# Kernel optimization log

Hardware: AMD Instinct MI355X
Metric: run time of the kernel (lower is better)

## Reference

```python
import jax, jax.numpy as jnp
import numpy as np

H = 256
NUM_CONVS = 4
NUM_GRAPHS = 1024
N_PER_GRAPH = 32
ORDER = 3
NUM_TYPES = 22  # len(utils.BOND_TYPES)
NUM_NOISE_LEVEL = 50
ANNEAL_POWER = 2.0


def _build_graph():
    # Chain molecules extended to order-3 neighbors (mimics extend_graph on a path graph):
    # for |i-j| in [1,ORDER]: edge_order=|i-j|, edge_type = bond type if order 1 else NUM_TYPES+order-1.
    n = N_PER_GRAPH
    i, j = np.meshgrid(np.arange(n), np.arange(n), indexing='ij')
    dist = np.abs(i - j)
    mask = (dist >= 1) & (dist <= ORDER)
    src_l, dst_l, eo = i[mask], j[mask], dist[mask]
    offs = np.arange(NUM_GRAPHS)[:, None] * n
    src = (src_l[None, :] + offs).reshape(-1)
    dst = (dst_l[None, :] + offs).reshape(-1)
    edge_order = np.tile(eo, NUM_GRAPHS)
    rng = np.random.default_rng(0)
    bond_t = rng.integers(1, 5, size=edge_order.shape)
    edge_type = np.where(edge_order == 1, bond_t, NUM_TYPES + edge_order - 1)
    node2graph = np.repeat(np.arange(NUM_GRAPHS), n)
    return src, dst, edge_type, node2graph


def setup_inputs() -> dict:
    key = jax.random.key(0)
    ks = jax.random.split(key, 24)
    src, dst, edge_type, node2graph = _build_graph()
    N, E = node2graph.shape[0], src.shape[0]
    w = lambda k, s: (jax.random.normal(k, s, jnp.float32) * 0.05)
    sigmas = jnp.asarray(np.exp(np.linspace(np.log(10.0), np.log(0.01), NUM_NOISE_LEVEL)), dtype=jnp.float32)
    return {
        'atom_type': jnp.asarray(np.random.default_rng(1).integers(0, 100, N), jnp.int32),
        'edge_index': jnp.asarray(np.stack([src, dst]), jnp.int32),
        'edge_type': jnp.asarray(edge_type, jnp.int32),
        'node2graph': jnp.asarray(node2graph, jnp.int32),
        'noise_level': jax.random.randint(ks[0], (NUM_GRAPHS,), 0, NUM_NOISE_LEVEL, jnp.int32),
        'pos': jax.random.normal(ks[1], (N, 3), jnp.float32) * 3.0,
        'd_noise': jax.random.normal(ks[2], (E, 1), jnp.float32),
        'sigmas': sigmas,
        'node_emb': w(ks[3], (100, H)), 'edge_emb': w(ks[4], (100, H)),
        'in_W1': w(ks[5], (1, H)), 'in_b1': w(ks[6], (H,)),
        'in_W2': w(ks[7], (H, H)), 'in_b2': w(ks[8], (H,)),
        'gin_W1': w(ks[9], (NUM_CONVS, H, H)), 'gin_b1': w(ks[10], (NUM_CONVS, H)),
        'gin_W2': w(ks[11], (NUM_CONVS, H, H)), 'gin_b2': w(ks[12], (NUM_CONVS, H)),
        'out_W1': w(ks[13], (2 * H, H)), 'out_b1': w(ks[14], (H,)),
        'out_W2': w(ks[15], (H, H // 2)), 'out_b2': w(ks[16], (H // 2,)),
        'out_W3': w(ks[17], (H // 2, 1)), 'out_b3': w(ks[18], (1,)),
    }


def reference(atom_type, edge_index, edge_type, node2graph, noise_level,
              pos, d_noise, sigmas, node_emb, edge_emb,
              in_W1, in_b1, in_W2, in_b2,
              gin_W1, gin_b1, gin_W2, gin_b2,
              out_W1, out_b1, out_W2, out_b2, out_W3, out_b3):
    N = pos.shape[0]
    G = noise_level.shape[0]
    row, col = edge_index[0], edge_index[1]
    edge2graph = node2graph[row]                                  # [E]
    d = jnp.linalg.norm(pos[row] - pos[col], axis=-1, keepdims=True)  # [E,1]
    used_sigmas = sigmas[noise_level][edge2graph][:, None]        # [E,1]
    perturbed_d = d + d_noise * used_sigmas
    target = -(perturbed_d - d) / used_sigmas ** 2
    # embeddings + input MLP (Linear-relu-Linear)
    node_attr = node_emb[atom_type]                               # [N,H]
    d_emb = jax.nn.relu(perturbed_d @ in_W1 + in_b1) @ in_W2 + in_b2
    edge_attr = d_emb * edge_emb[edge_type]                       # [E,H]
    # GIN with GINE convs: agg = sum_j relu(x_j + e_ij); out = MLP(x + agg); relu between convs; residual
    x = node_attr
    n_convs = gin_W1.shape[0]
    for k in range(n_convs):
        msg = jax.nn.relu(x[row] + edge_attr)                     # [E,H]
        agg = jax.ops.segment_sum(msg, col, num_segments=N)       # [N,H]
        h = jax.nn.relu((x + agg) @ gin_W1[k] + gin_b1[k]) @ gin_W2[k] + gin_b2[k]
        if k < n_convs - 1:
            h = jax.nn.relu(h)
        x = h + x  # short_cut
    # edge score head
    feat = jnp.concatenate([x[row] * x[col], edge_attr], axis=-1)  # [E,2H]
    s = jax.nn.relu(feat @ out_W1 + out_b1)
    s = jax.nn.relu(s @ out_W2 + out_b2)
    s = s @ out_W3 + out_b3                                       # [E,1]
    scores = (s / used_sigmas).reshape(-1)
    t = target.reshape(-1)
    loss_e = 0.5 * (scores - t) ** 2 * used_sigmas.reshape(-1) ** ANNEAL_POWER
    return jax.ops.segment_sum(loss_e, edge2graph, num_segments=G)  # [G]
```

## Files before the change

kernel.cpp:

```cpp
#include <hip/hip_runtime.h>
#include <math.h>

typedef unsigned int u32;
typedef __attribute__((ext_vector_type(8))) short bf16x8;
typedef __attribute__((ext_vector_type(4))) float f32x4;

#define MFMA16(a,b,c) __builtin_amdgcn_mfma_f32_16x16x32_bf16(a,b,c,0,0,0)

__device__ inline u32 bf16r(float x){
  u32 u = __float_as_uint(x);
  return (u + 0x7fffu + ((u >> 16) & 1u)) >> 16;
}
__device__ inline u32 pack2(float a, float b){ return bf16r(a) | (bf16r(b) << 16); }
__device__ inline uint4 pack8(const float* f){
  uint4 v; v.x = pack2(f[0],f[1]); v.y = pack2(f[2],f[3]);
  v.z = pack2(f[4],f[5]); v.w = pack2(f[6],f[7]); return v;
}
__device__ inline float bf2f(short s){ return __uint_as_float(((u32)(unsigned short)s) << 16); }

__device__ __forceinline__ void gload_lds16(const void* g, void* l){
  __builtin_amdgcn_global_load_lds((const __attribute__((address_space(1))) unsigned int*)g,
                                   (__attribute__((address_space(3))) unsigned int*)l,
                                   16, 0, 0);
}

__device__ __forceinline__ int frag_off(int f, int quad){
  return (f>>1)*64 + (f&1)*32 + ((quad ^ ((f>>1)&3))*8);
}

__device__ __forceinline__ int xg(int g, int r){ return g ^ ((r ^ (g>>3)) & 7); }

__global__ void k_cvtAll(const float* __restrict__ inW2, const float* __restrict__ gW1,
                         const float* __restrict__ gW2, const float* __restrict__ oW1,
                         const float* __restrict__ oW2,
                         short* __restrict__ w2t, short* __restrict__ gw1t,
                         short* __restrict__ gw2t, short* __restrict__ ow1t,
                         short* __restrict__ ow2t){
  int gidx = blockIdx.x*256 + threadIdx.x;
  const float* src; short* dst; int t, K8, Nf;
  if (gidx < 8192)      { src = inW2; dst = w2t; t = gidx; K8 = 32; Nf = 256; }
  else if (gidx < 40960){ int r = gidx-8192;  int c = r>>13; t = r&8191;
                          src = gW1 + (size_t)c*65536; dst = gw1t + (size_t)c*65536; K8 = 32; Nf = 256; }
  else if (gidx < 73728){ int r = gidx-40960; int c = r>>13; t = r&8191;
                          src = gW2 + (size_t)c*65536; dst = gw2t + (size_t)c*65536; K8 = 32; Nf = 256; }
  else if (gidx < 90112){ t = gidx-73728; src = oW1; dst = ow1t; K8 = 64; Nf = 256; }
  else if (gidx < 94208){ t = gidx-90112; src = oW2; dst = ow2t; K8 = 32; Nf = 128; }
  else return;
  int f = t / K8, c = t - f*K8;
  float v[8];
  #pragma unroll
  for (int j=0;j<8;j++) v[j] = src[(size_t)(c*8+j)*Nf + f];
  ((uint4*)dst)[t] = pack8(v);
}

__global__ void k_pre(const int* __restrict__ ei, const int* __restrict__ n2g,
                      const int* __restrict__ nl, const float* __restrict__ sigmas,
                      const float* __restrict__ pos, const float* __restrict__ dn, int E,
                      float* __restrict__ pd, int* __restrict__ cnt, int* __restrict__ inlist){
  int e = blockIdx.x*256 + threadIdx.x;
  if (e >= E) return;
  int r = ei[e], c = ei[E+e];
  float sg = sigmas[nl[n2g[r]]];
  float dx = pos[3*r]-pos[3*c], dy = pos[3*r+1]-pos[3*c+1], dz = pos[3*r+2]-pos[3*c+2];
  float d = sqrtf(dx*dx + dy*dy + dz*dz);
  pd[e] = d + dn[e]*sg;
  int slot = atomicAdd(&cnt[c], 1);
  if (slot < 8) inlist[c*8 + slot] = e;
}

__global__ __launch_bounds__(256) void k_attr(
    const float* __restrict__ pd, const float* __restrict__ W1, const float* __restrict__ b1,
    const short* __restrict__ W2t, const float* __restrict__ b2,
    const int* __restrict__ etype, const float* __restrict__ eemb,
    short* __restrict__ attr, int E)
{
  int tid = threadIdx.x;
  int base = blockIdx.x*64;
  int wv = tid>>6, lane = tid&63, quad = lane>>4, l15 = lane&15;
  float pdv[4];
  #pragma unroll
  for (int nt=0;nt<4;nt++) pdv[nt] = pd[base + nt*16 + l15];
  f32x4 acc[4][4];
  #pragma unroll
  for (int mt=0;mt<4;mt++) for (int nt=0;nt<4;nt++) acc[mt][nt] = (f32x4)0.f;
  #pragma unroll
  for (int s=0; s<8; s++){
    int k0 = s*32 + quad*8;
    float4 w1a = *(const float4*)(W1 + k0), w1b = *(const float4*)(W1 + k0 + 4);
    float4 b1a = *(const float4*)(b1 + k0), b1b = *(const float4*)(b1 + k0 + 4);
    bf16x8 a[4], b[4];
    #pragma unroll
    for (int mt=0;mt<4;mt++){
      int f = (wv*4+mt)*16 + l15;
      a[mt] = *(const bf16x8*)(W2t + (size_t)f*256 + k0);
    }
    #pragma unroll
    for (int nt=0;nt<4;nt++){
      float p = pdv[nt];
      float f[8] = {fmaxf(p*w1a.x+b1a.x,0.f), fmaxf(p*w1a.y+b1a.y,0.f),
                    fmaxf(p*w1a.z+b1a.z,0.f), fmaxf(p*w1a.w+b1a.w,0.f),
                    fmaxf(p*w1b.x+b1b.x,0.f), fmaxf(p*w1b.y+b1b.y,0.f),
                    fmaxf(p*w1b.z+b1b.z,0.f), fmaxf(p*w1b.w+b1b.w,0.f)};
      uint4 u = pack8(f);
      b[nt] = *(bf16x8*)&u;
    }
    #pragma unroll
    for (int mt=0;mt<4;mt++)
      #pragma unroll
      for (int nt=0;nt<4;nt++)
        acc[mt][nt] = MFMA16(a[mt], b[nt], acc[mt][nt]);
  }
  #pragma unroll
  for (int nt=0;nt<4;nt++){
    int e = base + nt*16 + l15;
    int et = etype[e];
    #pragma unroll
    for (int mt=0;mt<4;mt++){
      int f0 = (wv*4+mt)*16 + quad*4;
      float4 bb = *(const float4*)(b2 + f0);
      float4 em = *(const float4*)(eemb + (size_t)et*256 + f0);
      float v0 = (acc[mt][nt][0]+bb.x)*em.x, v1 = (acc[mt][nt][1]+bb.y)*em.y;
      float v2 = (acc[mt][nt][2]+bb.z)*em.z, v3 = (acc[mt][nt][3]+bb.w)*em.w;
      uint2 v; v.x = pack2(v0,v1); v.y = pack2(v2,v3);
      *(uint2*)(attr + (size_t)e*256 + f0) = v;
    }
  }
}

__global__ __launch_bounds__(512,2) void k_conv4(
    const int* __restrict__ at, const float* __restrict__ nemb,
    const short* __restrict__ attrS, const int* __restrict__ ei,
    const int* __restrict__ cnt, const int* __restrict__ inlist,
    const short* __restrict__ gw1t, const float* __restrict__ gb1,
    const short* __restrict__ gw2t, const float* __restrict__ gb2,
    short* __restrict__ xF)
{
  __shared__ float xls[32*256];
  __shared__ uint4 AlsV[32*32];
  __shared__ uint4 T1V [32*32];
  short* Als = (short*)AlsV;
  short* T1  = (short*)T1V;
  int tid = threadIdx.x;
  int nbase = blockIdx.x*32;
  int wv = tid>>6, lane = tid&63, quad = lane>>4, l15 = lane&15;
  int jl = tid>>4, ch = tid&15;
  int deg;
  int eid[8], rl[8];
  {
    int j = nbase + jl;
    deg = min(cnt[j], 8);
    #pragma unroll
    for (int s=0;s<8;s++){
      int e = (s < deg) ? inlist[j*8 + s] : 0;
      eid[s] = e;
      rl[s]  = (s < deg) ? (ei[e] - nbase) : 0;
    }
  }
  {
    int a = at[nbase + jl];
    const float4* src = (const float4*)nemb + (size_t)a*64 + ch*4;
    float* xrow = xls + jl*256;
    #pragma unroll
    for (int q=0;q<4;q++)
      *(float4*)(xrow + (xg(ch*4+q, jl)<<2)) = src[q];
  }
  __syncthreads();
  for (int c=0; c<4; c++){
    const short* W1t = gw1t + (size_t)c*65536;
    const short* W2t = gw2t + (size_t)c*65536;
    const float* b1 = gb1 + c*256;
    const float* b2 = gb2 + c*256;
    {
      float f[16];
      const float* xrow = xls + jl*256;
      #pragma unroll
      for (int q=0;q<4;q++){
        float4 v = *(const float4*)(xrow + (xg(ch*4+q, jl)<<2));
        f[q*4]=v.x; f[q*4+1]=v.y; f[q*4+2]=v.z; f[q*4+3]=v.w;
      }
      #pragma unroll
      for (int s=0; s<8; s++){
        if (s < deg){
          int r = rl[s];
          const float* xr = xls + r*256;
          const short* ar = attrS + (size_t)eid[s]*256 + ch*16;
          uint4 a4a = *(const uint4*)(ar);
          uint4 a4b = *(const uint4*)(ar + 8);
          u32 us[8] = {a4a.x,a4a.y,a4a.z,a4a.w, a4b.x,a4b.y,a4b.z,a4b.w};
          #pragma unroll
          for (int q=0;q<4;q++){
            float4 xv = *(const float4*)(xr + (xg(ch*4+q, r)<<2));
            u32 lo = us[2*q], hi = us[2*q+1];
            f[q*4]   += fmaxf(xv.x + __uint_as_float(lo<<16), 0.f);
            f[q*4+1] += fmaxf(xv.y + __uint_as_float(lo&0xffff0000u), 0.f);
            f[q*4+2] += fmaxf(xv.z + __uint_as_float(hi<<16), 0.f);
            f[q*4+3] += fmaxf(xv.w + __uint_as_float(hi&0xffff0000u), 0.f);
          }
        }
      }
      #pragma unroll
      for (int qq=0;qq<2;qq++){
        int cc = ch*2 + qq;
        *(uint4*)(Als + jl*256 + ((cc ^ (jl&7))*8)) = pack8(f + qq*8);
      }
    }
    __syncthreads();
    f32x4 acc[2][2];
    #pragma unroll
    for (int mt=0;mt<2;mt++) for (int nt=0;nt<2;nt++) acc[mt][nt] = (f32x4)0.f;
    #pragma unroll
    for (int s=0; s<8; s++){
      bf16x8 a[2], b[2];
      #pragma unroll
      for (int mt=0;mt<2;mt++)
        a[mt] = *(const bf16x8*)(W1t + (size_t)((wv*2+mt)*16 + l15)*256 + s*32 + quad*8);
      #pragma unroll
      for (int nt=0;nt<2;nt++){
        int n = nt*16 + l15; int cc = s*4 + quad;
        b[nt] = *(const bf16x8*)(Als + n*256 + ((cc ^ (n&7))*8));
      }
      #pragma unroll
      for (int mt=0;mt<2;mt++)
        #pragma unroll
        for (int nt=0;nt<2;nt++)
          acc[mt][nt] = MFMA16(a[mt], b[nt], acc[mt][nt]);
    }
    #pragma unroll
    for (int mt=0;mt<2;mt++){
      int f0 = (wv*2+mt)*16 + quad*4;
      float4 bb = *(const float4*)(b1 + f0);
      int cg = f0 >> 3, off = (quad&1)*4;
      #pragma unroll
      for (int nt=0;nt<2;nt++){
        int n = nt*16 + l15;
        float v0 = fmaxf(acc[mt][nt][0]+bb.x,0.f), v1 = fmaxf(acc[mt][nt][1]+bb.y,0.f);
        float v2 = fmaxf(acc[mt][nt][2]+bb.z,0.f), v3 = fmaxf(acc[mt][nt][3]+bb.w,0.f);
        uint2 v; v.x = pack2(v0,v1); v.y = pack2(v2,v3);
        *(uint2*)(T1 + n*256 + ((cg ^ (n&7))*8) + off) = v;
      }
    }
    __syncthreads();
    f32x4 acc2[2][2];
    #pragma unroll
    for (int mt=0;mt<2;mt++) for (int nt=0;nt<2;nt++) acc2[mt][nt] = (f32x4)0.f;
    #pragma unroll
    for (int s=0; s<8; s++){
      bf16x8 a[2], b[2];
      #pragma unroll
      for (int mt=0;mt<2;mt++)
        a[mt] = *(const bf16x8*)(W2t + (size_t)((wv*2+mt)*16 + l15)*256 + s*32 + quad*8);
      #pragma unroll
      for (int nt=0;nt<2;nt++){
        int n = nt*16 + l15; int cc = s*4 + quad;
        b[nt] = *(const bf16x8*)(T1 + n*256 + ((cc ^ (n&7))*8));
      }
      #pragma unroll
      for (int mt=0;mt<2;mt++)
        #pragma unroll
        for (int nt=0;nt<2;nt++)
          acc2[mt][nt] = MFMA16(a[mt], b[nt], acc2[mt][nt]);
    }
    #pragma unroll
    for (int mt=0;mt<2;mt++){
      int f0 = (wv*2+mt)*16 + quad*4;
      float4 bb = *(const float4*)(b2 + f0);
      int g = f0 >> 2;
      #pragma unroll
      for (int nt=0;nt<2;nt++){
        int n = nt*16 + l15;
        float* px = xls + n*256 + (xg(g, n)<<2);
        float4 xv = *(float4*)px;
        float h0 = acc2[mt][nt][0]+bb.x, h1 = acc2[mt][nt][1]+bb.y;
        float h2 = acc2[mt][nt][2]+bb.z, h3 = acc2[mt][nt][3]+bb.w;
        if (c < 3){ h0=fmaxf(h0,0.f); h1=fmaxf(h1,0.f); h2=fmaxf(h2,0.f); h3=fmaxf(h3,0.f); }
        xv.x += h0; xv.y += h1; xv.z += h2; xv.w += h3;
        *(float4*)px = xv;
      }
    }
    __syncthreads();
  }
  {
    const float* xrow = xls + jl*256;
    float f[16];
    #pragma unroll
    for (int q=0;q<4;q++){
      float4 v = *(const float4*)(xrow + (xg(ch*4+q, jl)<<2));
      f[q*4]=v.x; f[q*4+1]=v.y; f[q*4+2]=v.z; f[q*4+3]=v.w;
    }
    #pragma unroll
    for (int qq=0;qq<2;qq++)
      *(uint4*)(xF + (size_t)(nbase+jl)*256 + ch*16 + qq*8) = pack8(f + qq*8);
  }
}

__global__ __launch_bounds__(256,2) void k_head(
    const short* __restrict__ xF, const short* __restrict__ attrS,
    const int* __restrict__ ei,
    const short* __restrict__ W1t, const float* __restrict__ ob1,
    const short* __restrict__ W2t, const float* __restrict__ ob2,
    const float* __restrict__ W3, const float* __restrict__ ob3,
    const float* __restrict__ dnoise, const int* __restrict__ n2g,
    float* __restrict__ out, int E, int G)
{
  __shared__ uint4 BlsV[16*256];
  __shared__ float Sedge[64];
  __shared__ float part[4];
  short* Bls = (short*)BlsV;
  short* T   = (short*)BlsV;
  int tid = threadIdx.x;
  int base = blockIdx.x*64;
  int wv = tid>>6, lane = tid&63, quad = lane>>4, l15 = lane&15;
  if (tid < 64) Sedge[tid] = 0.f;
  if (tid < 4) part[tid] = 0.f;
  {
    int g = wv*64 + lane;
    int p = g>>3, hi = (g>>2)&1, cs = g&3;
    int n = p*2 + hi, cc = cs ^ (p&3);
    const short* srcb = attrS + (size_t)(base+n)*256 + cc*8;
    #pragma unroll
    for (int s=8; s<16; s++)
      gload_lds16(srcb + (s-8)*32, (char*)Bls + (size_t)s*4096 + wv*1024);
  }
  {
    int g = tid;
    int p = g>>3, hi = (g>>2)&1, cs = g&3;
    int n = p*2 + hi, cc = cs ^ (p&3);
    int rr = ei[base+n], rc = ei[E+base+n];
    const short* xr = xF + (size_t)rr*256 + cc*8;
    const short* xc = xF + (size_t)rc*256 + cc*8;
    #pragma unroll
    for (int s=0; s<8; s++){
      bf16x8 va = *(const bf16x8*)(xr + s*32);
      bf16x8 vb = *(const bf16x8*)(xc + s*32);
      float f[8];
      #pragma unroll
      for (int j=0;j<8;j++) f[j] = bf2f(va[j])*bf2f(vb[j]);
      *(uint4*)(Bls + (size_t)s*2048 + g*8) = pack8(f);
    }
  }
  __syncthreads();
  f32x4 acc[4][4];
  #pragma unroll
  for (int mt=0;mt<4;mt++) for (int nt=0;nt<4;nt++) acc[mt][nt] = (f32x4)0.f;
  #pragma unroll
  for (int s=0; s<16; s++){
    bf16x8 a[4], b[4];
    #pragma unroll
    for (int mt=0;mt<4;mt++)
      a[mt] = *(const bf16x8*)(W1t + (size_t)((wv*4+mt)*16 + l15)*512 + s*32 + quad*8);
    #pragma unroll
    for (int nt=0;nt<4;nt++)
      b[nt] = *(const bf16x8*)(Bls + (size_t)s*2048 + frag_off(nt*16 + l15, quad));
    #pragma unroll
    for (int mt=0;mt<4;mt++)
      #pragma unroll
      for (int nt=0;nt<4;nt++)
        acc[mt][nt] = MFMA16(a[mt], b[nt], acc[mt][nt]);
  }
  __syncthreads();
  #pragma unroll
  for (int mt=0;mt<4;mt++){
    int f0 = (wv*4+mt)*16 + quad*4;
    float4 bb = *(const float4*)(ob1 + f0);
    int c = f0 >> 3, off = (quad&1)*4;
    #pragma unroll
    for (int nt=0;nt<4;nt++){
      int n = nt*16 + l15;
      float v0 = fmaxf(acc[mt][nt][0]+bb.x,0.f), v1 = fmaxf(acc[mt][nt][1]+bb.y,0.f);
      float v2 = fmaxf(acc[mt][nt][2]+bb.z,0.f), v3 = fmaxf(acc[mt][nt][3]+bb.w,0.f);
      uint2 v; v.x = pack2(v0,v1); v.y = pack2(v2,v3);
      *(uint2*)(T + n*256 + ((c ^ (n&7))*8) + off) = v;
    }
  }
  __syncthreads();
  f32x4 acc2[2][4];
  #pragma unroll
  for (int mt=0;mt<2;mt++) for (int nt=0;nt<4;nt++) acc2[mt][nt] = (f32x4)0.f;
  #pragma unroll
  for (int s=0; s<8; s++){
    bf16x8 a[2], b[4];
    #pragma unroll
    for (int mt=0;mt<2;mt++)
      a[mt] = *(const bf16x8*)(W2t + (size_t)((wv*2+mt)*16 + l15)*256 + s*32 + quad*8);
    #pragma unroll
    for (int nt=0;nt<4;nt++){
      int n = nt*16 + l15; int cc = s*4 + quad;
      b[nt] = *(const bf16x8*)(T + n*256 + ((cc ^ (n&7))*8));
    }
    #pragma unroll
    for (int mt=0;mt<2;mt++)
      #pragma unroll
      for (int nt=0;nt<4;nt++)
        acc2[mt][nt] = MFMA16(a[mt], b[nt], acc2[mt][nt]);
  }
  float4 b2v[2], w3v[2];
  #pragma unroll
  for (int mt=0;mt<2;mt++){
    int f0 = (wv*2+mt)*16 + quad*4;
    b2v[mt] = *(const float4*)(ob2 + f0);
    w3v[mt] = *(const float4*)(W3 + f0);
  }
  #pragma unroll
  for (int nt=0;nt<4;nt++){
    float p = 0.f;
    #pragma unroll
    for (int mt=0;mt<2;mt++){
      p += fmaxf(acc2[mt][nt][0]+b2v[mt].x,0.f)*w3v[mt].x;
      p += fmaxf(acc2[mt][nt][1]+b2v[mt].y,0.f)*w3v[mt].y;
      p += fmaxf(acc2[mt][nt][2]+b2v[mt].z,0.f)*w3v[mt].z;
      p += fmaxf(acc2[mt][nt][3]+b2v[mt].w,0.f)*w3v[mt].w;
    }
    p += __shfl_xor(p, 16);
    p += __shfl_xor(p, 32);
    if (lane < 16) atomicAdd(&Sedge[nt*16 + l15], p);
  }
  __syncthreads();
  int gbase = n2g[ei[base]];
  if (tid < 64){
    int e = base + tid;
    float sv = Sedge[tid] + ob3[0] + dnoise[e];
    float l = 0.5f*sv*sv;
    int g = n2g[ei[e]] - gbase;
    atomicAdd(&part[g & 3], l);
  }
  __syncthreads();
  if (tid < 2 && (gbase + tid) < G)
    atomicAdd(&out[gbase + tid], part[tid]);
}

static inline size_t alignup(size_t v){ return (v + 255) & ~(size_t)255; }

extern "C" void kernel_launch(void* const* d_in, const int* in_sizes, int n_in,
                              void* d_out, int out_size, void* d_ws, size_t ws_size,
                              hipStream_t stream) {
  const int*   at    = (const int*)  d_in[0];
  const int*   ei    = (const int*)  d_in[1];
  const int*   etype = (const int*)  d_in[2];
  const int*   n2g   = (const int*)  d_in[3];
  const int*   nl    = (const int*)  d_in[4];
  const float* pos   = (const float*)d_in[5];
  const float* dnoi  = (const float*)d_in[6];
  const float* sig   = (const float*)d_in[7];
  const float* nemb  = (const float*)d_in[8];
  const float* eemb  = (const float*)d_in[9];
  const float* inW1  = (const float*)d_in[10];
  const float* inb1  = (const float*)d_in[11];
  const float* inW2  = (const float*)d_in[12];
  const float* inb2  = (const float*)d_in[13];
  const float* gW1   = (const float*)d_in[14];
  const float* gb1   = (const float*)d_in[15];
  const float* gW2   = (const float*)d_in[16];
  const float* gb2   = (const float*)d_in[17];
  const float* oW1   = (const float*)d_in[18];
  const float* ob1   = (const float*)d_in[19];
  const float* oW2   = (const float*)d_in[20];
  const float* ob2   = (const float*)d_in[21];
  const float* oW3   = (const float*)d_in[22];
  const float* ob3   = (const float*)d_in[23];
  float* out = (float*)d_out;

  const int N = in_sizes[0];
  const int E = in_sizes[2];
  const int G = in_sizes[4];
  const int H = 256;

  char* w = (char*)d_ws;
  size_t off = 0;
  size_t o_attr  = off; off = alignup(off + (size_t)E*H*2);
  size_t o_xF    = off; off = alignup(off + (size_t)N*H*2);
  size_t o_pd    = off; off = alignup(off + (size_t)E*4);
  size_t o_cnt   = off; off = alignup(off + (size_t)N*4);
  size_t o_inl   = off; off = alignup(off + (size_t)N*8*4);
  size_t o_w2t   = off; off = alignup(off + (size_t)H*H*2);
  size_t o_gw1t  = off; off = alignup(off + (size_t)4*H*H*2);
  size_t o_gw2t  = off; off = alignup(off + (size_t)4*H*H*2);
  size_t o_ow1t  = off; off = alignup(off + (size_t)H*2*H*2);
  size_t o_ow2t  = off; off = alignup(off + (size_t)(H/2)*H*2);
  (void)ws_size; (void)n_in; (void)out_size;

  short* attrS = (short*)(w + o_attr);
  short* xF    = (short*)(w + o_xF);
  float* pd    = (float*)(w + o_pd);
  int*   cnt   = (int*)  (w + o_cnt);
  int*   inl   = (int*)  (w + o_inl);
  short* w2t   = (short*)(w + o_w2t);
  short* gw1t  = (short*)(w + o_gw1t);
  short* gw2t  = (short*)(w + o_gw2t);
  short* ow1t  = (short*)(w + o_ow1t);
  short* ow2t  = (short*)(w + o_ow2t);

  hipMemsetAsync(cnt, 0, (size_t)N*4, stream);
  hipMemsetAsync(out, 0, (size_t)G*4, stream);

  k_cvtAll<<<368, 256, 0, stream>>>(inW2, gW1, gW2, oW1, oW2,
                                    w2t, gw1t, gw2t, ow1t, ow2t);

  k_pre<<<(E+255)/256, 256, 0, stream>>>(ei, n2g, nl, sig, pos, dnoi, E, pd, cnt, inl);
  k_attr<<<E/64, 256, 0, stream>>>(pd, inW1, inb1, w2t, inb2, etype, eemb, attrS, E);

  k_conv4<<<G, 512, 0, stream>>>(at, nemb, attrS, ei, cnt, inl,
                                 gw1t, gb1, gw2t, gb2, xF);

  k_head<<<E/64, 256, 0, stream>>>(xF, attrS, ei, ow1t, ob1, ow2t, ob2,
                                   oW3, ob3, dnoi, n2g, out, E, G);
}
```

Baseline: 507.0 us.

## Store conv node state as bf16 in LDS and double head block size

In the conv kernel, the per-node feature state held in shared memory changes from fp32 to bf16 with a new swizzle, which halves LDS use so three blocks can fit per CU (launch bounds raised to 3). The residual update now reads bf16, adds in fp32 and repacks, so rounding error builds up across the four convs. The head kernel moves from 256 to 512 threads, with each wave owning fewer output tiles and the tile loads split across the two halves. This is meant to raise occupancy and latency hiding, at the cost of lower precision in the carried node state.

Result: no change. 503.2 us (-0.8%).

```diff
diff --git a/kernel.cpp b/kernel.cpp
--- a/kernel.cpp
+++ b/kernel.cpp
@@ -28,7 +28,7 @@
   return (f>>1)*64 + (f&1)*32 + ((quad ^ ((f>>1)&3))*8);
 }
 
-__device__ __forceinline__ int xg(int g, int r){ return g ^ ((r ^ (g>>3)) & 7); }
+__device__ __forceinline__ int xg2(int g, int r){ return g ^ ((r ^ (g>>1)) & 7); }
 
 __global__ void k_cvtAll(const float* __restrict__ inW2, const float* __restrict__ gW1,
                          const float* __restrict__ gW2, const float* __restrict__ oW1,
@@ -127,7 +127,7 @@
   }
 }
 
-__global__ __launch_bounds__(512,2) void k_conv4(
+__global__ __launch_bounds__(512,3) void k_conv4(
     const int* __restrict__ at, const float* __restrict__ nemb,
     const short* __restrict__ attrS, const int* __restrict__ ei,
     const int* __restrict__ cnt, const int* __restrict__ inlist,
@@ -135,7 +135,7 @@
     const short* __restrict__ gw2t, const float* __restrict__ gb2,
     short* __restrict__ xF)
 {
-  __shared__ float xls[32*256];
+  __shared__ short xls[32*256];
   __shared__ uint4 AlsV[32*32];
   __shared__ uint4 T1V [32*32];
   short* Als = (short*)AlsV;
@@ -158,11 +158,15 @@
   }
   {
     int a = at[nbase + jl];
-    const float4* src = (const float4*)nemb + (size_t)a*64 + ch*4;
-    float* xrow = xls + jl*256;
-    #pragma unroll
-    for (int q=0;q<4;q++)
-      *(float4*)(xrow + (xg(ch*4+q, jl)<<2)) = src[q];
+    const float* src = nemb + (size_t)a*256 + ch*16;
+    float f[16];
+    #pragma unroll
+    for (int q=0;q<4;q++){
+      float4 v = *(const float4*)(src + q*4);
+      f[q*4]=v.x; f[q*4+1]=v.y; f[q*4+2]=v.z; f[q*4+3]=v.w;
+    }
+    *(uint4*)(xls + jl*256 + xg2(ch*2,   jl)*8) = pack8(f);
+    *(uint4*)(xls + jl*256 + xg2(ch*2+1, jl)*8) = pack8(f+8);
   }
   __syncthreads();
   for (int c=0; c<4; c++){
@@ -172,29 +176,25 @@
     const float* b2 = gb2 + c*256;
     {
       float f[16];
-      const float* xrow = xls + jl*256;
-      #pragma unroll
-      for (int q=0;q<4;q++){
-        float4 v = *(const float4*)(xrow + (xg(ch*4+q, jl)<<2));
-        f[q*4]=v.x; f[q*4+1]=v.y; f[q*4+2]=v.z; f[q*4+3]=v.w;
+      {
+        bf16x8 v0 = *(const bf16x8*)(xls + jl*256 + xg2(ch*2,   jl)*8);
+        bf16x8 v1 = *(const bf16x8*)(xls + jl*256 + xg2(ch*2+1, jl)*8);
+        #pragma unroll
+        for (int j=0;j<8;j++){ f[j]=bf2f(v0[j]); f[8+j]=bf2f(v1[j]); }
       }
       #pragma unroll
       for (int s=0; s<8; s++){
         if (s < deg){
           int r = rl[s];
-          const float* xr = xls + r*256;
+          bf16x8 x0 = *(const bf16x8*)(xls + r*256 + xg2(ch*2,   r)*8);
+          bf16x8 x1 = *(const bf16x8*)(xls + r*256 + xg2(ch*2+1, r)*8);
           const short* ar = attrS + (size_t)eid[s]*256 + ch*16;
-          uint4 a4a = *(const uint4*)(ar);
-          uint4 a4b = *(const uint4*)(ar + 8);
-          u32 us[8] = {a4a.x,a4a.y,a4a.z,a4a.w, a4b.x,a4b.y,a4b.z,a4b.w};
+          bf16x8 a0 = *(const bf16x8*)(ar);
+          bf16x8 a1 = *(const bf16x8*)(ar + 8);
           #pragma unroll
-          for (int q=0;q<4;q++){
-            float4 xv = *(const float4*)(xr + (xg(ch*4+q, r)<<2));
-            u32 lo = us[2*q], hi = us[2*q+1];
-            f[q*4]   += fmaxf(xv.x + __uint_as_float(lo<<16), 0.f);
-            f[q*4+1] += fmaxf(xv.y + __uint_as_float(lo&0xffff0000u), 0.f);
-            f[q*4+2] += fmaxf(xv.z + __uint_as_float(hi<<16), 0.f);
-            f[q*4+3] += fmaxf(xv.w + __uint_as_float(hi&0xffff0000u), 0.f);
+          for (int j=0;j<8;j++){
+            f[j]   += fmaxf(bf2f(x0[j]) + bf2f(a0[j]), 0.f);
+            f[8+j] += fmaxf(bf2f(x1[j]) + bf2f(a1[j]), 0.f);
           }
         }
       }
@@ -264,36 +264,32 @@
     for (int mt=0;mt<2;mt++){
       int f0 = (wv*2+mt)*16 + quad*4;
       float4 bb = *(const float4*)(b2 + f0);
-      int g = f0 >> 2;
+      int g2 = f0 >> 3, half = (quad&1)*4;
       #pragma unroll
       for (int nt=0;nt<2;nt++){
         int n = nt*16 + l15;
-        float* px = xls + n*256 + (xg(g, n)<<2);
-        float4 xv = *(float4*)px;
+        short* px = xls + n*256 + xg2(g2, n)*8 + half;
+        uint2 old = *(uint2*)px;
+        float o0 = __uint_as_float(old.x<<16), o1 = __uint_as_float(old.x&0xffff0000u);
+        float o2 = __uint_as_float(old.y<<16), o3 = __uint_as_float(old.y&0xffff0000u);
         float h0 = acc2[mt][nt][0]+bb.x, h1 = acc2[mt][nt][1]+bb.y;
         float h2 = acc2[mt][nt][2]+bb.z, h3 = acc2[mt][nt][3]+bb.w;
         if (c < 3){ h0=fmaxf(h0,0.f); h1=fmaxf(h1,0.f); h2=fmaxf(h2,0.f); h3=fmaxf(h3,0.f); }
-        xv.x += h0; xv.y += h1; xv.z += h2; xv.w += h3;
-        *(float4*)px = xv;
+        uint2 v; v.x = pack2(o0+h0, o1+h1); v.y = pack2(o2+h2, o3+h3);
+        *(uint2*)px = v;
       }
     }
     __syncthreads();
   }
   {
-    const float* xrow = xls + jl*256;
-    float f[16];
-    #pragma unroll
-    for (int q=0;q<4;q++){
-      float4 v = *(const float4*)(xrow + (xg(ch*4+q, jl)<<2));
-      f[q*4]=v.x; f[q*4+1]=v.y; f[q*4+2]=v.z; f[q*4+3]=v.w;
-    }
-    #pragma unroll
-    for (int qq=0;qq<2;qq++)
-      *(uint4*)(xF + (size_t)(nbase+jl)*256 + ch*16 + qq*8) = pack8(f + qq*8);
-  }
-}
-
-__global__ __launch_bounds__(256,2) void k_head(
+    uint4 v0 = *(const uint4*)(xls + jl*256 + xg2(ch*2,   jl)*8);
+    uint4 v1 = *(const uint4*)(xls + jl*256 + xg2(ch*2+1, jl)*8);
+    *(uint4*)(xF + (size_t)(nbase+jl)*256 + ch*16)     = v0;
+    *(uint4*)(xF + (size_t)(nbase+jl)*256 + ch*16 + 8) = v1;
+  }
+}
+
+__global__ __launch_bounds__(512,2) void k_head(
     const short* __restrict__ xF, const short* __restrict__ attrS,
     const int* __restrict__ ei,
     const short* __restrict__ W1t, const float* __restrict__ ob1,
@@ -312,55 +308,57 @@
   int wv = tid>>6, lane = tid&63, quad = lane>>4, l15 = lane&15;
   if (tid < 64) Sedge[tid] = 0.f;
   if (tid < 4) part[tid] = 0.f;
-  {
-    int g = wv*64 + lane;
-    int p = g>>3, hi = (g>>2)&1, cs = g&3;
+  int g8 = tid & 255, sh = tid >> 8, w4 = g8 >> 6;
+  {
+    int p = g8>>3, hi = (g8>>2)&1, cs = g8&3;
     int n = p*2 + hi, cc = cs ^ (p&3);
     const short* srcb = attrS + (size_t)(base+n)*256 + cc*8;
     #pragma unroll
-    for (int s=8; s<16; s++)
-      gload_lds16(srcb + (s-8)*32, (char*)Bls + (size_t)s*4096 + wv*1024);
-  }
-  {
-    int g = tid;
-    int p = g>>3, hi = (g>>2)&1, cs = g&3;
+    for (int i=0;i<4;i++){
+      int s = 8 + i*2 + sh;
+      gload_lds16(srcb + (s-8)*32, (char*)BlsV + (size_t)s*4096 + w4*1024);
+    }
+  }
+  {
+    int p = g8>>3, hi = (g8>>2)&1, cs = g8&3;
     int n = p*2 + hi, cc = cs ^ (p&3);
     int rr = ei[base+n], rc = ei[E+base+n];
     const short* xr = xF + (size_t)rr*256 + cc*8;
     const short* xc = xF + (size_t)rc*256 + cc*8;
     #pragma unroll
-    for (int s=0; s<8; s++){
+    for (int i=0;i<4;i++){
+      int s = sh*4 + i;
       bf16x8 va = *(const bf16x8*)(xr + s*32);
       bf16x8 vb = *(const bf16x8*)(xc + s*32);
       float f[8];
       #pragma unroll
       for (int j=0;j<8;j++) f[j] = bf2f(va[j])*bf2f(vb[j]);
-      *(uint4*)(Bls + (size_t)s*2048 + g*8) = pack8(f);
-    }
-  }
-  __syncthreads();
-  f32x4 acc[4][4];
-  #pragma unroll
-  for (int mt=0;mt<4;mt++) for (int nt=0;nt<4;nt++) acc[mt][nt] = (f32x4)0.f;
+      *(uint4*)(Bls + (size_t)s*2048 + g8*8) = pack8(f);
+    }
+  }
+  __syncthreads();
+  f32x4 acc[2][4];
+  #pragma unroll
+  for (int mt=0;mt<2;mt++) for (int nt=0;nt<4;nt++) acc[mt][nt] = (f32x4)0.f;
   #pragma unroll
   for (int s=0; s<16; s++){
-    bf16x8 a[4], b[4];
-    #pragma unroll
-    for (int mt=0;mt<4;mt++)
-      a[mt] = *(const bf16x8*)(W1t + (size_t)((wv*4+mt)*16 + l15)*512 + s*32 + quad*8);
+    bf16x8 a[2], b[4];
+    #pragma unroll
+    for (int mt=0;mt<2;mt++)
+      a[mt] = *(const bf16x8*)(W1t + (size_t)((wv*2+mt)*16 + l15)*512 + s*32 + quad*8);
     #pragma unroll
     for (int nt=0;nt<4;nt++)
       b[nt] = *(const bf16x8*)(Bls + (size_t)s*2048 + frag_off(nt*16 + l15, quad));
     #pragma unroll
-    for (int mt=0;mt<4;mt++)
+    for (int mt=0;mt<2;mt++)
       #pragma unroll
       for (int nt=0;nt<4;nt++)
         acc[mt][nt] = MFMA16(a[mt], b[nt], acc[mt][nt]);
   }
   __syncthreads();
   #pragma unroll
-  for (int mt=0;mt<4;mt++){
-    int f0 = (wv*4+mt)*16 + quad*4;
+  for (int mt=0;mt<2;mt++){
+    int f0 = (wv*2+mt)*16 + quad*4;
     float4 bb = *(const float4*)(ob1 + f0);
     int c = f0 >> 3, off = (quad&1)*4;
     #pragma unroll
@@ -373,46 +371,31 @@
     }
   }
   __syncthreads();
-  f32x4 acc2[2][4];
-  #pragma unroll
-  for (int mt=0;mt<2;mt++) for (int nt=0;nt<4;nt++) acc2[mt][nt] = (f32x4)0.f;
+  f32x4 acc2[4];
+  #pragma unroll
+  for (int nt=0;nt<4;nt++) acc2[nt] = (f32x4)0.f;
   #pragma unroll
   for (int s=0; s<8; s++){
-    bf16x8 a[2], b[4];
-    #pragma unroll
-    for (int mt=0;mt<2;mt++)
-      a[mt] = *(const bf16x8*)(W2t + (size_t)((wv*2+mt)*16 + l15)*256 + s*32 + quad*8);
+    bf16x8 a = *(const bf16x8*)(W2t + (size_t)(wv*16 + l15)*256 + s*32 + quad*8);
     #pragma unroll
     for (int nt=0;nt<4;nt++){
       int n = nt*16 + l15; int cc = s*4 + quad;
-      b[nt] = *(const bf16x8*)(T + n*256 + ((cc ^ (n&7))*8));
-    }
-    #pragma unroll
-    for (int mt=0;mt<2;mt++)
-      #pragma unroll
-      for (int nt=0;nt<4;nt++)
-        acc2[mt][nt] = MFMA16(a[mt], b[nt], acc2[mt][nt]);
-  }
-  float4 b2v[2], w3v[2];
-  #pragma unroll
-  for (int mt=0;mt<2;mt++){
-    int f0 = (wv*2+mt)*16 + quad*4;
-    b2v[mt] = *(const float4*)(ob2 + f0);
-    w3v[mt] = *(const float4*)(W3 + f0);
-  }
-  #pragma unroll
-  for (int nt=0;nt<4;nt++){
-    float p = 0.f;
-    #pragma unroll
-    for (int mt=0;mt<2;mt++){
-      p += fmaxf(acc2[mt][nt][0]+b2v[mt].x,0.f)*w3v[mt].x;
-      p += fmaxf(acc2[mt][nt][1]+b2v[mt].y,0.f)*w3v[mt].y;
-      p += fmaxf(acc2[mt][nt][2]+b2v[mt].z,0.f)*w3v[mt].z;
-      p += fmaxf(acc2[mt][nt][3]+b2v[mt].w,0.f)*w3v[mt].w;
-    }
-    p += __shfl_xor(p, 16);
-    p += __shfl_xor(p, 32);
-    if (lane < 16) atomicAdd(&Sedge[nt*16 + l15], p);
+      bf16x8 b = *(const bf16x8*)(T + n*256 + ((cc ^ (n&7))*8));
+      acc2[nt] = MFMA16(a, b, acc2[nt]);
+    }
+  }
+  {
+    int f0 = wv*16 + quad*4;
+    float4 bb = *(const float4*)(ob2 + f0);
+    float4 w3 = *(const float4*)(W3 + f0);
+    #pragma unroll
+    for (int nt=0;nt<4;nt++){
+      float p = fmaxf(acc2[nt][0]+bb.x,0.f)*w3.x + fmaxf(acc2[nt][1]+bb.y,0.f)*w3.y
+              + fmaxf(acc2[nt][2]+bb.z,0.f)*w3.z + fmaxf(acc2[nt][3]+bb.w,0.f)*w3.w;
+      p += __shfl_xor(p, 16);
+      p += __shfl_xor(p, 32);
+      if (lane < 16) atomicAdd(&Sedge[nt*16 + l15], p);
+    }
   }
   __syncthreads();
   int gbase = n2g[ei[base]];
@@ -501,6 +484,6 @@
   k_conv4<<<G, 512, 0, stream>>>(at, nemb, attrS, ei, cnt, inl,
                                  gw1t, gb1, gw2t, gb2, xF);
 
-  k_head<<<E/64, 256, 0, stream>>>(xF, attrS, ei, ow1t, ob1, ow2t, ob2,
+  k_head<<<E/64, 512, 0, stream>>>(xF, attrS, ei, ow1t, ob1, ow2t, ob2,
                                    oW3, ob3, dnoi, n2g, out, E, G);
 }
```
